# Performance work log

Measured on AMD Instinct MI355X. Metric: run time of the kernel, lower is better.

Reference implementation:

```python
import jax, jax.numpy as jnp
import numpy as np
import math

IN_DIM = 3
WIDTH = 256
DEPTH = 6
OUT_DIM = 1
W0_FIRST = 30.0
W0_HIDDEN = 1.0
N_POINTS = 1048576


def _uniform(key, shape, bound):
    return jax.random.uniform(key, shape, dtype=jnp.float32, minval=-bound, maxval=bound)


def setup_inputs() -> dict:
    key = jax.random.key(0)
    ks = jax.random.split(key, 8)
    xyt = jax.random.uniform(ks[0], (N_POINTS, IN_DIM), dtype=jnp.float32, minval=-1.0, maxval=1.0)
    # first layer: bound = 1/in_features
    W0 = _uniform(ks[1], (WIDTH, IN_DIM), 1.0 / IN_DIM)
    b0 = jnp.zeros((WIDTH,), jnp.float32)
    # hidden layers: bound = sqrt(6/width)/w0_hidden
    hb = math.sqrt(6.0 / WIDTH) / W0_HIDDEN
    W1 = _uniform(ks[2], (WIDTH, WIDTH), hb)
    b1 = jnp.zeros((WIDTH,), jnp.float32)
    W2 = _uniform(ks[3], (WIDTH, WIDTH), hb)
    b2 = jnp.zeros((WIDTH,), jnp.float32)
    W3 = _uniform(ks[4], (WIDTH, WIDTH), hb)
    b3 = jnp.zeros((WIDTH,), jnp.float32)
    W4 = _uniform(ks[5], (WIDTH, WIDTH), hb)
    b4 = jnp.zeros((WIDTH,), jnp.float32)
    Wf = _uniform(ks[6], (OUT_DIM, WIDTH), hb)
    bf = jnp.zeros((OUT_DIM,), jnp.float32)
    return {"xyt": xyt, "W0": W0, "b0": b0, "W1": W1, "b1": b1,
            "W2": W2, "b2": b2, "W3": W3, "b3": b3, "W4": W4, "b4": b4,
            "Wf": Wf, "bf": bf}


def reference(xyt, W0, b0, W1, b1, W2, b2, W3, b3, W4, b4, Wf, bf):
    # SineLayer: sin(w0 * (x @ W^T + b)); torch Linear weight is [out, in]
    h = jnp.sin(W0_FIRST * (xyt @ W0.T + b0))          # [N, 256]
    for W, b in ((W1, b1), (W2, b2), (W3, b3), (W4, b4)):
        h = jnp.sin(W0_HIDDEN * (h @ W.T + b))          # [N, 256]
    out = h @ Wf.T + bf                                  # [N, 1]
    return out.squeeze(-1)                               # [N]
```

## Files before the change

kernel.cpp:

```cpp
#include <hip/hip_runtime.h>

typedef _Float16 half8 __attribute__((ext_vector_type(8)));
typedef _Float16 half4 __attribute__((ext_vector_type(4)));
typedef float f32x4 __attribute__((ext_vector_type(4)));

#define WPAD 264
#define NPB 64
#define THREADS 256

__global__ void convert_weights(const float* __restrict__ W1, const float* __restrict__ W2,
                                const float* __restrict__ W3, const float* __restrict__ W4,
                                _Float16* __restrict__ Wc) {
    int tid = blockIdx.x * 256 + threadIdx.x;
    int l   = tid >> 16;
    int rem = tid & 65535;
    int n = rem >> 8, k = rem & 255;
    const float* W = (l == 0) ? W1 : (l == 1) ? W2 : (l == 2) ? W3 : W4;
    int kc = k >> 5, kl = k & 31;
    Wc[l * 65536 + kc * 8192 + n * 32 + kl] = (_Float16)W[rem];
}

__launch_bounds__(THREADS, 2)
__global__ void siren_fused(const float* __restrict__ xyt,
                            const float* __restrict__ W0,
                            const float* __restrict__ b0,
                            const _Float16* __restrict__ Wc,
                            const float* __restrict__ b1,
                            const float* __restrict__ b2,
                            const float* __restrict__ b3,
                            const float* __restrict__ b4,
                            const float* __restrict__ Wf,
                            const float* __restrict__ bfin,
                            float* __restrict__ out)
{
    __shared__ _Float16 hbuf[NPB * WPAD];
    __shared__ float    xs[NPB * 3];
    __shared__ float    wf_s[256];

    const int tid  = threadIdx.x;
    const int lane = tid & 63;
    const int wv   = tid >> 6;
    const int l15  = lane & 15;
    const int l4   = lane >> 4;
    const int gm0  = blockIdx.x * NPB;

    if (tid < NPB * 3) xs[tid] = xyt[gm0 * 3 + tid];
    wf_s[tid] = Wf[tid];
    __syncthreads();

    {
        const int n = tid;
        const float w0x = W0[n * 3], w0y = W0[n * 3 + 1], w0z = W0[n * 3 + 2];
        const float bb = b0[n];
        #pragma unroll 8
        for (int m = 0; m < NPB; ++m) {
            float z = 30.0f * fmaf(w0x, xs[m * 3],
                          fmaf(w0y, xs[m * 3 + 1],
                          fmaf(w0z, xs[m * 3 + 2], bb)));
            hbuf[m * WPAD + n] = (_Float16)__sinf(z);
        }
    }

    const int arow = (wv * 64 + l15) * 32 + l4 * 8;

    half8 areg[4][4];
    {
        const _Float16* wl = Wc;
        #pragma unroll
        for (int c = 0; c < 4; ++c)
            #pragma unroll
            for (int i = 0; i < 4; ++i)
                areg[c][i] = *(const half8*)&wl[c * 8192 + arow + i * 512];
    }

    #pragma unroll
    for (int l = 0; l < 4; ++l) {
        const float* bl = (l == 0) ? b1 : (l == 1) ? b2 : (l == 2) ? b3 : b4;

        __syncthreads();

        half8 bfr[4][8];
        #pragma unroll
        for (int j = 0; j < 4; ++j)
            #pragma unroll
            for (int c = 0; c < 8; ++c)
                bfr[j][c] = *(const half8*)&hbuf[(j * 16 + l15) * WPAD + c * 32 + l4 * 8];

        __syncthreads();

        f32x4 acc[4][4];
        #pragma unroll
        for (int i = 0; i < 4; ++i)
            #pragma unroll
            for (int j = 0; j < 4; ++j)
                acc[i][j] = (f32x4){0.f, 0.f, 0.f, 0.f};

        const _Float16* wl = Wc + l * 65536;
        #pragma unroll
        for (int kc = 0; kc < 8; ++kc) {
            #pragma unroll
            for (int i = 0; i < 4; ++i) {
                half8 af = areg[kc & 3][i];
                #pragma unroll
                for (int j = 0; j < 4; ++j)
                    acc[i][j] = __builtin_amdgcn_mfma_f32_16x16x32_f16(af, bfr[j][kc], acc[i][j], 0, 0, 0);
            }
            if (kc < 4) {
                #pragma unroll
                for (int i = 0; i < 4; ++i)
                    areg[kc & 3][i] = *(const half8*)&wl[(kc + 4) * 8192 + arow + i * 512];
            }
        }

        if (l < 3) {
            const _Float16* wn = Wc + (l + 1) * 65536;
            #pragma unroll
            for (int c = 0; c < 4; ++c)
                #pragma unroll
                for (int i = 0; i < 4; ++i)
                    areg[c][i] = *(const half8*)&wn[c * 8192 + arow + i * 512];
        }

        #pragma unroll
        for (int i = 0; i < 4; ++i) {
            f32x4 bb = ((const f32x4*)bl)[wv * 16 + i * 4 + l4];
            #pragma unroll
            for (int j = 0; j < 4; ++j) {
                half4 hv;
                #pragma unroll
                for (int r = 0; r < 4; ++r)
                    hv[r] = (_Float16)__sinf(acc[i][j][r] + bb[r]);
                *(half4*)&hbuf[(j * 16 + l15) * WPAD + wv * 64 + i * 16 + l4 * 4] = hv;
            }
        }
    }

    __syncthreads();

    {
        const int m = tid >> 2, q = tid & 3;
        const _Float16* hrow = &hbuf[m * WPAD + q * 64];
        float sum = 0.f;
        #pragma unroll
        for (int i = 0; i < 8; ++i) {
            half8 hv = *(const half8*)&hrow[i * 8];
            const int nb = q * 64 + i * 8;
            #pragma unroll
            for (int j = 0; j < 8; ++j)
                sum = fmaf((float)hv[j], wf_s[nb + j], sum);
        }
        sum += __shfl_down(sum, 2);
        sum += __shfl_down(sum, 1);
        if (q == 0) out[gm0 + m] = sum + bfin[0];
    }
}

extern "C" void kernel_launch(void* const* d_in, const int* in_sizes, int n_in,
                              void* d_out, int out_size, void* d_ws, size_t ws_size,
                              hipStream_t stream) {
    const float* xyt = (const float*)d_in[0];
    const float* W0  = (const float*)d_in[1];
    const float* b0  = (const float*)d_in[2];
    const float* W1  = (const float*)d_in[3];
    const float* b1  = (const float*)d_in[4];
    const float* W2  = (const float*)d_in[5];
    const float* b2  = (const float*)d_in[6];
    const float* W3  = (const float*)d_in[7];
    const float* b3  = (const float*)d_in[8];
    const float* W4  = (const float*)d_in[9];
    const float* b4  = (const float*)d_in[10];
    const float* Wf  = (const float*)d_in[11];
    const float* bf  = (const float*)d_in[12];
    float* out = (float*)d_out;
    _Float16* Wc = (_Float16*)d_ws;

    convert_weights<<<1024, 256, 0, stream>>>(W1, W2, W3, W4, Wc);

    const int N = in_sizes[0] / 3;
    siren_fused<<<N / NPB, THREADS, 0, stream>>>(
        xyt, W0, b0, Wc, b1, b2, b3, b4, Wf, bf, out);
}
```

Before: 730.0 us.

## Retile SIREN MLP to 128 points × 8 waves and fold 1/2π into weights

Each block now handles 128 points with 512 threads, and each wave owns 32 output features across all 128 points. Weight fragments are streamed per k-chunk with a one-step prefetch, and activation fragments are read from LDS per k-chunk, instead of keeping a large register-resident A/B set. The 1/(2π) factor is folded into the converted weights, the biases and the first-layer scale so the raw hardware sin builtin, which takes its argument in revolutions, can be used directly. The bias is also used to initialise the accumulators. This aims to cut register pressure, raise occupancy and remove sin range reduction, at the cost of about 70KB of dynamic LDS per block and more LDS traffic.

```diff
diff --git a/kernel.cpp b/kernel.cpp
--- a/kernel.cpp
+++ b/kernel.cpp
@@ -5,8 +5,11 @@
 typedef float f32x4 __attribute__((ext_vector_type(4)));
 
 #define WPAD 264
-#define NPB 64
-#define THREADS 256
+#define NPB 128
+#define THREADS 512
+#define INV2PI 0.15915494309189535f
+#define W0SCALE (30.0f * INV2PI)
+#define SMEM_BYTES (NPB * WPAD * 2 + (384 + 256) * 4)
 
 __global__ void convert_weights(const float* __restrict__ W1, const float* __restrict__ W2,
                                 const float* __restrict__ W3, const float* __restrict__ W4,
@@ -17,10 +20,10 @@
     int n = rem >> 8, k = rem & 255;
     const float* W = (l == 0) ? W1 : (l == 1) ? W2 : (l == 2) ? W3 : W4;
     int kc = k >> 5, kl = k & 31;
-    Wc[l * 65536 + kc * 8192 + n * 32 + kl] = (_Float16)W[rem];
+    Wc[l * 65536 + kc * 8192 + n * 32 + kl] = (_Float16)(W[rem] * INV2PI);
 }
 
-__launch_bounds__(THREADS, 2)
+__launch_bounds__(THREADS, 4)
 __global__ void siren_fused(const float* __restrict__ xyt,
                             const float* __restrict__ W0,
                             const float* __restrict__ b0,
@@ -33,9 +36,10 @@
                             const float* __restrict__ bfin,
                             float* __restrict__ out)
 {
-    __shared__ _Float16 hbuf[NPB * WPAD];
-    __shared__ float    xs[NPB * 3];
-    __shared__ float    wf_s[256];
+    extern __shared__ _Float16 smem[];
+    _Float16* hbuf = smem;
+    float* xs   = (float*)(smem + NPB * WPAD);
+    float* wf_s = xs + 384;
 
     const int tid  = threadIdx.x;
     const int lane = tid & 63;
@@ -44,95 +48,97 @@
     const int l4   = lane >> 4;
     const int gm0  = blockIdx.x * NPB;
 
-    if (tid < NPB * 3) xs[tid] = xyt[gm0 * 3 + tid];
-    wf_s[tid] = Wf[tid];
+    if (tid < 384) xs[tid] = xyt[gm0 * 3 + tid];
+    if (tid < 256) wf_s[tid] = Wf[tid];
     __syncthreads();
 
     {
-        const int n = tid;
-        const float w0x = W0[n * 3], w0y = W0[n * 3 + 1], w0z = W0[n * 3 + 2];
-        const float bb = b0[n];
-        #pragma unroll 8
-        for (int m = 0; m < NPB; ++m) {
-            float z = 30.0f * fmaf(w0x, xs[m * 3],
-                          fmaf(w0y, xs[m * 3 + 1],
-                          fmaf(w0z, xs[m * 3 + 2], bb)));
-            hbuf[m * WPAD + n] = (_Float16)__sinf(z);
+        const int fg = lane;
+        const int p0 = wv * 16;
+        float w[4][3], bb[4];
+        #pragma unroll
+        for (int c = 0; c < 4; ++c) {
+            const int n = fg * 4 + c;
+            w[c][0] = W0[n * 3 + 0] * W0SCALE;
+            w[c][1] = W0[n * 3 + 1] * W0SCALE;
+            w[c][2] = W0[n * 3 + 2] * W0SCALE;
+            bb[c]   = b0[n] * W0SCALE;
+        }
+        #pragma unroll 4
+        for (int p = 0; p < 16; ++p) {
+            const float x0 = xs[(p0 + p) * 3], x1 = xs[(p0 + p) * 3 + 1], x2 = xs[(p0 + p) * 3 + 2];
+            half4 hv;
+            #pragma unroll
+            for (int c = 0; c < 4; ++c) {
+                float z = fmaf(w[c][0], x0, fmaf(w[c][1], x1, fmaf(w[c][2], x2, bb[c])));
+                hv[c] = (_Float16)__builtin_amdgcn_sinf(z);
+            }
+            *(half4*)&hbuf[(p0 + p) * WPAD + fg * 4] = hv;
         }
     }
 
-    const int arow = (wv * 64 + l15) * 32 + l4 * 8;
-
-    half8 areg[4][4];
-    {
-        const _Float16* wl = Wc;
-        #pragma unroll
-        for (int c = 0; c < 4; ++c)
-            #pragma unroll
-            for (int i = 0; i < 4; ++i)
-                areg[c][i] = *(const half8*)&wl[c * 8192 + arow + i * 512];
-    }
+    const int arow = (wv * 32 + l15) * 32 + l4 * 8;
 
     #pragma unroll
     for (int l = 0; l < 4; ++l) {
         const float* bl = (l == 0) ? b1 : (l == 1) ? b2 : (l == 2) ? b3 : b4;
+        const _Float16* wl = Wc + l * 65536;
+
+        half8 areg[2][2];
+        #pragma unroll
+        for (int c = 0; c < 2; ++c)
+            #pragma unroll
+            for (int i = 0; i < 2; ++i)
+                areg[c][i] = *(const half8*)&wl[c * 8192 + arow + i * 512];
+
+        f32x4 acc[2][8];
+        #pragma unroll
+        for (int i = 0; i < 2; ++i) {
+            f32x4 bb = *(const f32x4*)&bl[wv * 32 + i * 16 + l4 * 4];
+            bb *= INV2PI;
+            #pragma unroll
+            for (int j = 0; j < 8; ++j)
+                acc[i][j] = bb;
+        }
 
         __syncthreads();
 
-        half8 bfr[4][8];
         #pragma unroll
-        for (int j = 0; j < 4; ++j)
+        for (int kc = 0; kc < 8; ++kc) {
+            half8 anext[2];
+            if (kc < 6) {
+                #pragma unroll
+                for (int i = 0; i < 2; ++i)
+                    anext[i] = *(const half8*)&wl[(kc + 2) * 8192 + arow + i * 512];
+            }
             #pragma unroll
-            for (int c = 0; c < 8; ++c)
-                bfr[j][c] = *(const half8*)&hbuf[(j * 16 + l15) * WPAD + c * 32 + l4 * 8];
+            for (int g = 0; g < 2; ++g) {
+                half8 bfr[4];
+                #pragma unroll
+                for (int j = 0; j < 4; ++j)
+                    bfr[j] = *(const half8*)&hbuf[((g * 4 + j) * 16 + l15) * WPAD + kc * 32 + l4 * 8];
+                #pragma unroll
+                for (int i = 0; i < 2; ++i)
+                    #pragma unroll
+                    for (int j = 0; j < 4; ++j)
+                        acc[i][g * 4 + j] = __builtin_amdgcn_mfma_f32_16x16x32_f16(
+                            areg[kc & 1][i], bfr[j], acc[i][g * 4 + j], 0, 0, 0);
+            }
+            if (kc < 6) { areg[kc & 1][0] = anext[0]; areg[kc & 1][1] = anext[1]; }
+        }
 
         __syncthreads();
 
-        f32x4 acc[4][4];
         #pragma unroll
-        for (int i = 0; i < 4; ++i)
+        for (int i = 0; i < 2; ++i)
             #pragma unroll
-            for (int j = 0; j < 4; ++j)
-                acc[i][j] = (f32x4){0.f, 0.f, 0.f, 0.f};
-
-        const _Float16* wl = Wc + l * 65536;
-        #pragma unroll
-        for (int kc = 0; kc < 8; ++kc) {
-            #pragma unroll
-            for (int i = 0; i < 4; ++i) {
-                half8 af = areg[kc & 3][i];
-                #pragma unroll
-                for (int j = 0; j < 4; ++j)
-                    acc[i][j] = __builtin_amdgcn_mfma_f32_16x16x32_f16(af, bfr[j][kc], acc[i][j], 0, 0, 0);
-            }
-            if (kc < 4) {
-                #pragma unroll
-                for (int i = 0; i < 4; ++i)
-                    areg[kc & 3][i] = *(const half8*)&wl[(kc + 4) * 8192 + arow + i * 512];
-            }
-        }
-
-        if (l < 3) {
-            const _Float16* wn = Wc + (l + 1) * 65536;
-            #pragma unroll
-            for (int c = 0; c < 4; ++c)
-                #pragma unroll
-                for (int i = 0; i < 4; ++i)
-                    areg[c][i] = *(const half8*)&wn[c * 8192 + arow + i * 512];
-        }
-
-        #pragma unroll
-        for (int i = 0; i < 4; ++i) {
-            f32x4 bb = ((const f32x4*)bl)[wv * 16 + i * 4 + l4];
-            #pragma unroll
-            for (int j = 0; j < 4; ++j) {
+            for (int j = 0; j < 8; ++j) {
                 half4 hv;
                 #pragma unroll
                 for (int r = 0; r < 4; ++r)
-                    hv[r] = (_Float16)__sinf(acc[i][j][r] + bb[r]);
-                *(half4*)&hbuf[(j * 16 + l15) * WPAD + wv * 64 + i * 16 + l4 * 4] = hv;
+                    hv[r] = (_Float16)__builtin_amdgcn_sinf(acc[i][j][r]);
+                *(half4*)&hbuf[(j * 16 + l15) * WPAD + wv * 32 + i * 16 + l4 * 4] = hv;
             }
-        }
     }
 
     __syncthreads();
@@ -174,9 +180,12 @@
     float* out = (float*)d_out;
     _Float16* Wc = (_Float16*)d_ws;
 
+    hipFuncSetAttribute((const void*)siren_fused,
+                        hipFuncAttributeMaxDynamicSharedMemorySize, SMEM_BYTES);
+
     convert_weights<<<1024, 256, 0, stream>>>(W1, W2, W3, W4, Wc);
 
     const int N = in_sizes[0] / 3;
-    siren_fused<<<N / NPB, THREADS, 0, stream>>>(
+    siren_fused<<<N / NPB, THREADS, SMEM_BYTES, stream>>>(
         xyt, W0, b0, Wc, b1, b2, b3, b4, Wf, bf, out);
 }
```

New measurement: 620.6 us. 1.18x faster.
